# Kernel tuning notes

Measured on AMD Instinct MI355X. Metric: run time of the kernel, lower is better.

## Reference

```python
import jax, jax.numpy as jnp
import numpy as np

B, C, T = 256, 22, 1000          # batch, EEG channels, samples
NB, M, E, K = 6, 8, 6, 3         # nbands, m, num_experts, top_k
KERNELS = (3, 5, 7)
FS = 250
POOL = FS // 2                   # 125
NUM_CLASSES = 9
EPS = 1e-5
NUM_TAPS = 21


def _firwin_bp(numtaps, f1, f2, fs):
    """scipy.signal.firwin(numtaps,[f1,f2],pass_zero=False,fs=fs) with Hamming window."""
    nyq = fs / 2.0
    lo, hi = f1 / nyq, f2 / nyq
    m = np.arange(numtaps) - (numtaps - 1) / 2.0
    h = hi * np.sinc(hi * m) - lo * np.sinc(lo * m)
    h = h * np.hamming(numtaps)
    h = h / np.sum(h * np.cos(np.pi * m * (lo + hi) / 2.0))  # unit gain at band center
    return h.astype(np.float32)


def setup_inputs() -> dict:
    key = jax.random.key(0)
    ks = jax.random.split(key, 10)
    fir = np.stack([_firwin_bp(NUM_TAPS, lo, lo + 4, FS) for lo in range(8, 32, 4)])  # (6,21)
    return {
        "x": jax.random.normal(ks[0], (B, C, T), jnp.float32),
        "fir_kernels": jnp.asarray(fir),
        "pconv_w3": jax.random.normal(ks[1], (NB, 1, 1, 3), jnp.float32) * 0.3,
        "pconv_w5": jax.random.normal(ks[2], (NB, 1, 1, 5), jnp.float32) * 0.3,
        "pconv_w7": jax.random.normal(ks[3], (NB, 1, 1, 7), jnp.float32) * 0.3,
        "bn1_g": jnp.ones((NB,), jnp.float32),
        "bn1_b": jnp.zeros((NB,), jnp.float32),
        "bn1_m": jnp.zeros((NB,), jnp.float32),
        "bn1_v": jnp.ones((NB,), jnp.float32),
        "sconv_w": jax.random.normal(ks[4], (NB, 1, C, 1), jnp.float32) * 0.2,
        "gate_w": jax.random.normal(ks[5], (M * NB, NB), jnp.float32) * 0.4,
        "gate_b": jnp.zeros((M * NB,), jnp.float32),
        "exp_w": jax.random.normal(ks[6], (E, M * NB, NB), jnp.float32) * 0.3,
        "exp_b": jnp.zeros((E, M * NB), jnp.float32),
        "ebn_g": jnp.ones((E, M * NB), jnp.float32),
        "ebn_b": jnp.zeros((E, M * NB), jnp.float32),
        "ebn_m": jnp.zeros((E, M * NB), jnp.float32),
        "ebn_v": jnp.ones((E, M * NB), jnp.float32),
        "fc_w": jax.random.normal(ks[7], (NUM_CLASSES, M * NB * (T // POOL)), jnp.float32) * 0.05,
        "fc_b": jnp.zeros((NUM_CLASSES,), jnp.float32),
    }


def _forward(x, fir_kernels, pconv_w3, pconv_w5, pconv_w7, bn1_g, bn1_b, bn1_m, bn1_v,
             sconv_w, gate_w, gate_b, exp_w, exp_b, ebn_g, ebn_b, ebn_m, ebn_v, fc_w, fc_b):
    Bsz = x.shape[0]
    pad = NUM_TAPS // 2
    # --- FIR filterbank: depthwise conv1d, channel-multiplier = NB bands ---
    rhs = jnp.broadcast_to(fir_kernels[None, :, None, :], (C, NB, 1, NUM_TAPS)).reshape(C * NB, 1, NUM_TAPS)
    xb = jax.lax.conv_general_dilated(x, rhs, (1,), [(pad, pad)],
                                      dimension_numbers=("NCH", "OIH", "NCH"), feature_group_count=C)
    xb = xb.reshape(Bsz, C, NB, T).transpose(0, 2, 1, 3)  # (B, NB, C, T)
    # --- parallel depthwise (1,k) convs, concat along time, avgpool(1, nk) ---
    outs = []
    for w in (pconv_w3, pconv_w5, pconv_w7):
        k = w.shape[-1]
        outs.append(jax.lax.conv_general_dilated(xb, w, (1, 1), [(0, 0), (k // 2, k // 2)],
                                                 dimension_numbers=("NCHW", "OIHW", "NCHW"),
                                                 feature_group_count=NB))
    h = jnp.concatenate(outs, axis=-1)                       # (B, NB, C, nk*T)
    nk = len(KERNELS)
    h = h.reshape(Bsz, NB, C, h.shape[-1] // nk, nk).mean(-1)  # (B, NB, C, T)
    # --- sconv: BN2d(eval) + ReLU + (dropout=identity in eval) + depthwise (C,1) conv ---
    scale1 = bn1_g / jnp.sqrt(bn1_v + EPS)
    h = (h - bn1_m[None, :, None, None]) * scale1[None, :, None, None] + bn1_b[None, :, None, None]
    h = jax.nn.relu(h)
    h = jax.lax.conv_general_dilated(h, sconv_w, (1, 1), [(0, 0), (0, 0)],
                                     dimension_numbers=("NCHW", "OIHW", "NCHW"), feature_group_count=NB)
    h = h[:, :, 0, :]                                        # squeeze -> (B, NB, T)
    # --- MoE: gate over M*NB logits, top-k mask (no grad), only first E cols mix experts ---
    gw = jax.nn.softmax(h.mean(-1) @ gate_w.T + gate_b, axis=-1)  # (B, M*NB)
    _, idx = jax.lax.top_k(gw, K)
    mask = jnp.zeros_like(gw).at[jnp.arange(Bsz)[:, None], idx].set(1.0)
    mask = jax.lax.stop_gradient(mask)
    gw = gw * mask
    gw = gw / gw.sum(-1, keepdims=True)
    # dense experts: 1x1 conv + avgpool(POOL) + BN1d(eval) + ReLU, vectorized over experts
    y = jnp.einsum("bct,eoc->beot", h, exp_w) + exp_b[None, :, :, None]   # (B, E, M*NB, T)
    y = y.reshape(Bsz, E, M * NB, T // POOL, POOL).mean(-1)               # (B, E, M*NB, T//POOL)
    escale = ebn_g / jnp.sqrt(ebn_v + EPS)
    y = (y - ebn_m[None, :, :, None]) * escale[None, :, :, None] + ebn_b[None, :, :, None]
    y = jax.nn.relu(y)
    out = jnp.einsum("be,beot->bot", gw[:, :E], y)                        # (B, M*NB, T//POOL)
    feats = out.reshape(Bsz, -1)                                          # (B, 384)
    logp = jax.nn.log_softmax(feats @ fc_w.T + fc_b, axis=1)              # (B, 9)
    return feats, logp


def reference(x, fir_kernels, pconv_w3, pconv_w5, pconv_w7, bn1_g, bn1_b, bn1_m, bn1_v,
              sconv_w, gate_w, gate_b, exp_w, exp_b, ebn_g, ebn_b, ebn_m, ebn_v, fc_w, fc_b):
    return _forward(x, fir_kernels, pconv_w3, pconv_w5, pconv_w7, bn1_g, bn1_b, bn1_m, bn1_v,
                    sconv_w, gate_w, gate_b, exp_w, exp_b, ebn_g, ebn_b, ebn_m, ebn_v, fc_w, fc_b)
```

## Files before the change

### kernel.cpp

```cpp
#include <hip/hip_runtime.h>
#include <math.h>

#define B_    256
#define C_    22
#define T_    1000
#define NB_   6
#define E_    6
#define MNB_  48
#define POOL_ 125
#define TP_   8
#define NC_   9
#define FEAT_ 384

#define PQ_   352
#define NTH   768
#define CH_   11

#define PASS(OFF, KK)                                                        \
    {                                                                        \
        float f[16];                                                         \
        const float4* pb = (const float4*)(base + (OFF));                    \
        *(float4*)&f[0]  = pb[0]; *(float4*)&f[4]  = pb[1];                  \
        *(float4*)&f[8]  = pb[2]; *(float4*)&f[12] = pb[3];                  \
        _Pragma("unroll")                                                    \
        for (int u = 0; u < 13; ++u) {                                       \
            const float cj = ck2[KK][u];                                     \
            s0 = fmaf(cj, f[u    ], s0);                                     \
            s1 = fmaf(cj, f[u + 1], s1);                                     \
            s2 = fmaf(cj, f[u + 2], s2);                                     \
            s3 = fmaf(cj, f[u + 3], s3);                                     \
        }                                                                    \
    }

#define RUN_NB(NBV, A0, A1, A2, A3)                                          \
    {                                                                        \
        const int nbL = (NBV);                                               \
        float ck2[3][13];                                                    \
        _Pragma("unroll")                                                    \
        for (int k = 0; k < 3; ++k)                                          \
            _Pragma("unroll")                                                \
            for (int u = 0; u < 13; ++u) ck2[k][u] = ckl2[rr][nbL][k][u];    \
        const float sc3 = sbn6[nbL][0], bi = sbn6[nbL][1];                   \
        _Pragma("unroll 1")                                                  \
        for (int c = 0; c < CH_; ++c) {                                      \
            const float* base = &pl[c][0][0];                                \
            float s0 = 0.f, s1 = 0.f, s2 = 0.f, s3 = 0.f;                    \
            PASS(off0, 0)                                                    \
            PASS(off1, 1)                                                    \
            PASS(off2, 2)                                                    \
            const float sw = sws6[nbL][h * CH_ + c];                         \
            A0 += fmaxf(fmaf(s0, sc3, bi), 0.f) * sw;                        \
            A1 += fmaxf(fmaf(s1, sc3, bi), 0.f) * sw;                        \
            A2 += fmaxf(fmaf(s2, sc3, bi), 0.f) * sw;                        \
            A3 += fmaxf(fmaf(s3, sc3, bi), 0.f) * sw;                        \
        }                                                                    \
    }

__global__ __launch_bounds__(NTH) void fb_fused(
    const float* __restrict__ x,
    const float* __restrict__ fir,
    const float* __restrict__ w3,
    const float* __restrict__ w5,
    const float* __restrict__ w7,
    const float* __restrict__ bn_g, const float* __restrict__ bn_b,
    const float* __restrict__ bn_m, const float* __restrict__ bn_v,
    const float* __restrict__ sconv_w,
    const float* __restrict__ gate_w, const float* __restrict__ gate_b,
    const float* __restrict__ exp_w,  const float* __restrict__ exp_b,
    const float* __restrict__ ebn_g,  const float* __restrict__ ebn_b,
    const float* __restrict__ ebn_m,  const float* __restrict__ ebn_v,
    const float* __restrict__ fc_w,   const float* __restrict__ fc_b,
    float* __restrict__ feats_out, float* __restrict__ logp_out)
{
    const int b   = blockIdx.x;
    const int tid = threadIdx.x;

    __shared__ __align__(16) float pl[CH_][3][PQ_];
    __shared__ float firs6[NB_][21];
    __shared__ float w3s6[NB_][3], w5s6[NB_][5], w7s6[NB_][7];
    __shared__ float sws6[NB_][C_];
    __shared__ float sbn6[NB_][2];
    __shared__ float ckl2[3][NB_][3][13];
    __shared__ float xbv[NB_][CH_][13];
    __shared__ float term[NB_][6][C_];
    __shared__ float corr[NB_][6];
    __shared__ float psum[MNB_];
    __shared__ float hpl[MNB_];
    __shared__ float gms[NB_];
    __shared__ float lg[MNB_];
    __shared__ float gsh[E_];
    __shared__ float fsh[FEAT_];
    __shared__ float fpart[NC_][8];
    __shared__ float lo[NC_];

    float (*hrow)[T_] = (float (*)[T_])pl;

    const float* xbase = x + (size_t)b * (C_ * T_);

    if (tid < 126)                      { int nb=tid/21; firs6[nb][tid%21] = fir[tid]; }
    else if (tid >= 128 && tid < 146)   { int k=tid-128; w3s6[k/3][k%3] = w3[k]; }
    else if (tid >= 160 && tid < 190)   { int k=tid-160; w5s6[k/5][k%5] = w5[k]; }
    else if (tid >= 192 && tid < 234)   { int k=tid-192; w7s6[k/7][k%7] = w7[k]; }
    else if (tid >= 256 && tid < 388)   { int k=tid-256; sws6[k/C_][k%C_] = sconv_w[k]; }
    else if (tid >= 400 && tid < 406) {
        const int nb = tid - 400;
        float sc = bn_g[nb] * rsqrtf(bn_v[nb] + 1e-5f);
        sbn6[nb][0] = sc * (1.f/3.f);
        sbn6[nb][1] = bn_b[nb] - bn_m[nb] * sc;
    }

    const bool act  = (tid < 750);
    const int  tile = act ? (tid % 250) : 0;
    const int  nbA  = act ? (tid / 250) : 0;
    const int  nbB  = nbA + 3;
    const int  rr   = (tile <= 82) ? 0 : (tile <= 166) ? 1 : 2;

    const int PLN[3][3]  = {{2,0,1},{1,2,0},{0,1,2}};
    const int AOFF[3][3] = {{0,4,4},{-332,-332,-332},{-664,-664,-664}};
    const int off0 = PLN[rr][0]*PQ_ + 4*tile + AOFF[rr][0];
    const int off1 = PLN[rr][1]*PQ_ + 4*tile + AOFF[rr][1];
    const int off2 = PLN[rr][2]*PQ_ + 4*tile + AOFF[rr][2];

    float aA0=0.f, aA1=0.f, aA2=0.f, aA3=0.f;
    float aB0=0.f, aB1=0.f, aB2=0.f, aB3=0.f;

    #pragma unroll 1
    for (int h = 0; h < 2; ++h) {
        #pragma unroll
        for (int k = 0; k < 4; ++k) {
            const int idx = tid + k * NTH;
            if (idx < CH_ * 264) {
                const int cl = idx / 264, r2 = idx % 264;
                const int p  = r2 / 88,  q0 = (r2 % 88) * 4;
                const float* xr = xbase + (h * CH_ + cl) * T_;
                float v[4];
                #pragma unroll
                for (int i = 0; i < 4; ++i) {
                    const int m  = 3 * (q0 + i) + p - 24;
                    const int mc = m < 0 ? 0 : (m > 999 ? 999 : m);
                    const float val = xr[mc];
                    v[i] = ((unsigned)m < 1000u) ? val : 0.f;
                }
                *(float4*)&pl[cl][p][q0] = make_float4(v[0], v[1], v[2], v[3]);
            }
        }
        __syncthreads();

        if (h == 0 && tid < 702) {
            const int rr2 = tid / 234, r234 = tid % 234;
            const int nb  = r234 / 39, r39 = r234 % 39;
            const int k   = r39 / 13,  u   = r39 % 13;
            const int IDX0[3][3] = {{3,0,0},{2,2,3},{1,1,1}};
            const int jj = k + 3*u - 3*IDX0[rr2][k];
            float s = 0.f;
            if (jj >= 0 && jj < 29) {
                const float* wk = (rr2 == 0) ? w3s6[nb] : (rr2 == 1 ? w5s6[nb] : w7s6[nb]);
                const int K = (rr2 == 0) ? 3 : (rr2 == 1 ? 5 : 7), pk = K >> 1;
                #pragma unroll
                for (int oi = 0; oi < 9; ++oi) {
                    const int o = oi - 3;
                    float we = 0.f;
                    for (int kk = 0; kk < 7; ++kk) {
                        if (kk < K) {
                            const int jx = o + pk - kk;
                            if (jx >= 0 && jx < 3) we += wk[kk];
                        }
                    }
                    const int i = jj - oi;
                    if (i >= 0 && i < 21) s = fmaf(we, firs6[nb][i], s);
                }
            }
            ckl2[rr2][nb][k][u] = s;
        }
        for (int idx = tid; idx < NB_ * CH_ * 13; idx += NTH) {
            const int nb = idx / (CH_ * 13), r143 = idx % (CH_ * 13);
            const int cl = r143 / 13, pos = r143 % 13;
            const int m  = (pos < 7) ? pos : (987 + pos);
            int mm = m + 14;
            int q  = mm / 3, p = mm - 3 * q;
            float s = 0.f;
            #pragma unroll
            for (int i = 0; i < 21; ++i) {
                s = fmaf(firs6[nb][i], pl[cl][p][q], s);
                ++p; if (p == 3) { p = 0; ++q; }
            }
            xbv[nb][cl][pos] = s;
        }
        __syncthreads();

        if (tid < NB_ * 6 * CH_) {
            const int nb  = tid / (6 * CH_), r66 = tid % (6 * CH_);
            const int tix = r66 / CH_, cl = r66 % CH_;
            const float* X  = xbv[nb][cl];
            const float* W3 = w3s6[nb];
            const float* W5 = w5s6[nb];
            const float* W7 = w7s6[nb];
            float s;
            switch (tix) {
            case 0:
                s = W3[1]*X[0]+W3[2]*X[1]
                  + W3[0]*X[0]+W3[1]*X[1]+W3[2]*X[2]
                  + W3[0]*X[1]+W3[1]*X[2]+W3[2]*X[3];
                break;
            case 1:
                s = W3[0]*X[8]+W3[1]*X[9]+W3[2]*X[10]
                  + W3[0]*X[9]+W3[1]*X[10]+W3[2]*X[11]
                  + W3[0]*X[10]+W3[1]*X[11]+W3[2]*X[12];
                break;
            case 2:
                s = W3[0]*X[11]+W3[1]*X[12]
                  + W5[2]*X[0]+W5[3]*X[1]+W5[4]*X[2]
                  + W5[1]*X[0]+W5[2]*X[1]+W5[3]*X[2]+W5[4]*X[3];
                break;
            case 3:
                s = W5[0]*X[9]+W5[1]*X[10]+W5[2]*X[11]+W5[3]*X[12]
                  + W5[0]*X[10]+W5[1]*X[11]+W5[2]*X[12]
                  + W7[3]*X[0]+W7[4]*X[1]+W7[5]*X[2]+W7[6]*X[3];
                break;
            case 4:
                s = W7[2]*X[0]+W7[3]*X[1]+W7[4]*X[2]+W7[5]*X[3]+W7[6]*X[4]
                  + W7[1]*X[0]+W7[2]*X[1]+W7[3]*X[2]+W7[4]*X[3]+W7[5]*X[4]+W7[6]*X[5]
                  + W7[0]*X[0]+W7[1]*X[1]+W7[2]*X[2]+W7[3]*X[3]+W7[4]*X[4]+W7[5]*X[5]+W7[6]*X[6];
                break;
            default:
                s = W7[0]*X[7]+W7[1]*X[8]+W7[2]*X[9]+W7[3]*X[10]+W7[4]*X[11]+W7[5]*X[12]
                  + W7[0]*X[8]+W7[1]*X[9]+W7[2]*X[10]+W7[3]*X[11]+W7[4]*X[12]
                  + W7[0]*X[9]+W7[1]*X[10]+W7[2]*X[11]+W7[3]*X[12];
                break;
            }
            const float v = fmaxf(fmaf(s, sbn6[nb][0], sbn6[nb][1]), 0.f);
            term[nb][tix][h * CH_ + cl] = v * sws6[nb][h * CH_ + cl];
        }

        if (act) {
            RUN_NB(nbA, aA0, aA1, aA2, aA3)
            RUN_NB(nbB, aB0, aB1, aB2, aB3)
        }
        __syncthreads();
    }

    if (act) {
        *(float4*)&hrow[nbA][4*tile] = make_float4(aA0, aA1, aA2, aA3);
        *(float4*)&hrow[nbB][4*tile] = make_float4(aB0, aB1, aB2, aB3);
    }
    if (tid >= 704 && tid < 740) {
        const int k = tid - 704;
        const int nb = k / 6, tix = k % 6;
        float s = 0.f;
        for (int c = 0; c < C_; ++c) s += term[nb][tix][c];
        corr[nb][tix] = s;
    }
    __syncthreads();
    if (tid < 36) {
        const int nb = tid / 6, tix = tid % 6;
        const int t = (tix == 0) ? 0 :
                      (tix <= 2) ? (331 + tix) :
                      (tix <= 4) ? (663 + tix) : 999;
        hrow[nb][t] = corr[nb][tix];
    }
    __syncthreads();

    if (tid < 384) {
        const int w = tid >> 3, jj = tid & 7;
        const int nb = w >> 3, p = w & 7;
        float s = 0.f;
        for (int k = jj; k < POOL_; k += 8) s += hrow[nb][p*POOL_ + k];
        s += __shfl_down(s, 4, 8);
        s += __shfl_down(s, 2, 8);
        s += __shfl_down(s, 1, 8);
        if (jj == 0) { psum[w] = s; hpl[w] = s * (1.f / POOL_); }
    }
    __syncthreads();
    if (tid < NB_) {
        float s = 0.f;
        for (int p = 0; p < TP_; ++p) s += psum[tid*TP_ + p];
        gms[tid] = s * (1.f / T_);
    }
    __syncthreads();

    if (tid < MNB_) {
        float s = gate_b[tid];
        for (int c = 0; c < NB_; ++c) s += gms[c] * gate_w[tid*NB_ + c];
        lg[tid] = s;
    }
    __syncthreads();
    if (tid == 0) {
        float mx = lg[0];
        for (int i = 1; i < MNB_; ++i) mx = fmaxf(mx, lg[i]);
        for (int i = 0; i < MNB_; ++i) lg[i] = expf(lg[i] - mx);
        int i1 = 0, i2 = -1, i3 = -1;
        float b1 = -1.f, b2 = -1.f, b3 = -1.f;
        for (int i = 0; i < MNB_; ++i) if (lg[i] > b1) { b1 = lg[i]; i1 = i; }
        for (int i = 0; i < MNB_; ++i) if (i != i1 && lg[i] > b2) { b2 = lg[i]; i2 = i; }
        for (int i = 0; i < MNB_; ++i) if (i != i1 && i != i2 && lg[i] > b3) { b3 = lg[i]; i3 = i; }
        const float s3 = lg[i1] + lg[i2] + lg[i3];
        for (int jj = 0; jj < E_; ++jj) gsh[jj] = 0.f;
        if (i1 < E_) gsh[i1] = lg[i1] / s3;
        if (i2 < E_) gsh[i2] = lg[i2] / s3;
        if (i3 < E_) gsh[i3] = lg[i3] / s3;
    }
    __syncthreads();

    if (tid < FEAT_) {
        const int o = tid >> 3, p = tid & 7;
        float outv = 0.f;
        #pragma unroll
        for (int e = 0; e < E_; ++e) {
            const int eo = e*MNB_ + o;
            float acc = exp_b[eo];
            #pragma unroll
            for (int c = 0; c < NB_; ++c)
                acc += hpl[c*TP_ + p] * exp_w[eo*NB_ + c];
            const float esc = ebn_g[eo] * rsqrtf(ebn_v[eo] + 1e-5f);
            float v = fmaf(acc - ebn_m[eo], esc, ebn_b[eo]);
            v = fmaxf(v, 0.f);
            outv += gsh[e] * v;
        }
        fsh[tid] = outv;
        feats_out[b*FEAT_ + tid] = outv;
    }
    __syncthreads();

    if (tid < NC_ * 8) {
        const int cls = tid >> 3, part = tid & 7;
        float s = 0.f;
        const float* wr = fc_w + cls*FEAT_ + part*48;
        const float* fr = fsh + part*48;
        for (int i = 0; i < 48; ++i) s = fmaf(fr[i], wr[i], s);
        fpart[cls][part] = s;
    }
    __syncthreads();
    if (tid < NC_) {
        float s = fc_b[tid];
        for (int p = 0; p < 8; ++p) s += fpart[tid][p];
        lo[tid] = s;
    }
    __syncthreads();
    if (tid == 0) {
        float mx = lo[0];
        for (int k = 1; k < NC_; ++k) mx = fmaxf(mx, lo[k]);
        float Z = 0.f;
        for (int k = 0; k < NC_; ++k) Z += expf(lo[k] - mx);
        const float lse = mx + logf(Z);
        for (int k = 0; k < NC_; ++k) logp_out[b*NC_ + k] = lo[k] - lse;
    }
}

extern "C" void kernel_launch(void* const* d_in, const int* in_sizes, int n_in,
                              void* d_out, int out_size, void* d_ws, size_t ws_size,
                              hipStream_t stream) {
    const float* x       = (const float*)d_in[0];
    const float* fir     = (const float*)d_in[1];
    const float* w3      = (const float*)d_in[2];
    const float* w5      = (const float*)d_in[3];
    const float* w7      = (const float*)d_in[4];
    const float* bn1_g   = (const float*)d_in[5];
    const float* bn1_b   = (const float*)d_in[6];
    const float* bn1_m   = (const float*)d_in[7];
    const float* bn1_v   = (const float*)d_in[8];
    const float* sconv_w = (const float*)d_in[9];
    const float* gate_w  = (const float*)d_in[10];
    const float* gate_b  = (const float*)d_in[11];
    const float* exp_w   = (const float*)d_in[12];
    const float* exp_b   = (const float*)d_in[13];
    const float* ebn_g   = (const float*)d_in[14];
    const float* ebn_b   = (const float*)d_in[15];
    const float* ebn_m   = (const float*)d_in[16];
    const float* ebn_v   = (const float*)d_in[17];
    const float* fc_w    = (const float*)d_in[18];
    const float* fc_b    = (const float*)d_in[19];

    float* out       = (float*)d_out;
    float* feats_out = out;
    float* logp_out  = out + B_ * FEAT_;

    fb_fused<<<B_, NTH, 0, stream>>>(x, fir, w3, w5, w7,
                                     bn1_g, bn1_b, bn1_m, bn1_v, sconv_w,
                                     gate_w, gate_b, exp_w, exp_b,
                                     ebn_g, ebn_b, ebn_m, ebn_v,
                                     fc_w, fc_b, feats_out, logp_out);
}
```

Measured before the change: 62.88 us.

## Trim zero-padded taps and make thread-to-tile mapping wavefront-uniform per region

Replaces the padded 3x13 per-plane coefficient layout with a compact 29-tap array and unrolls only the nonzero taps per plane (10/10/9 instead of 13/13/13), cutting the FMA count in the inner convolution loop. Thread mapping is changed so each group of 256 threads handles one region (rr), making the rr branch uniform across wavefronts and letting the compiler specialize the loads with constant offsets. This adds three code paths, which raises code size and possibly register use.

```diff
diff --git a/kernel.cpp b/kernel.cpp
--- a/kernel.cpp
+++ b/kernel.cpp
@@ -16,39 +16,49 @@
 #define NTH   768
 #define CH_   11
 
-#define PASS(OFF, KK)                                                        \
+#define LOADP(F, pp, Aoff)                                                   \
     {                                                                        \
-        float f[16];                                                         \
-        const float4* pb = (const float4*)(base + (OFF));                    \
-        *(float4*)&f[0]  = pb[0]; *(float4*)&f[4]  = pb[1];                  \
-        *(float4*)&f[8]  = pb[2]; *(float4*)&f[12] = pb[3];                  \
-        _Pragma("unroll")                                                    \
-        for (int u = 0; u < 13; ++u) {                                       \
-            const float cj = ck2[KK][u];                                     \
-            s0 = fmaf(cj, f[u    ], s0);                                     \
-            s1 = fmaf(cj, f[u + 1], s1);                                     \
-            s2 = fmaf(cj, f[u + 2], s2);                                     \
-            s3 = fmaf(cj, f[u + 3], s3);                                     \
-        }                                                                    \
+        const float4* pb = (const float4*)&bw[pp][4*tile + (Aoff)];          \
+        *(float4*)&F[0]  = pb[0]; *(float4*)&F[4]  = pb[1];                  \
+        *(float4*)&F[8]  = pb[2]; *(float4*)&F[12] = pb[3];                  \
+    }
+
+#define TAPS(F, idx0, j0, nj)                                                \
+    _Pragma("unroll")                                                        \
+    for (int a = 0; a < (nj); ++a) {                                         \
+        const float cj = ck[(j0) + 3*a];                                     \
+        s0 = fmaf(cj, F[(idx0) + a    ], s0);                                \
+        s1 = fmaf(cj, F[(idx0) + a + 1], s1);                                \
+        s2 = fmaf(cj, F[(idx0) + a + 2], s2);                                \
+        s3 = fmaf(cj, F[(idx0) + a + 3], s3);                                \
     }
 
 #define RUN_NB(NBV, A0, A1, A2, A3)                                          \
     {                                                                        \
-        const int nbL = (NBV);                                               \
-        float ck2[3][13];                                                    \
+        const int nbL_ = (NBV);                                              \
+        float ck[29];                                                        \
         _Pragma("unroll")                                                    \
-        for (int k = 0; k < 3; ++k)                                          \
-            _Pragma("unroll")                                                \
-            for (int u = 0; u < 13; ++u) ck2[k][u] = ckl2[rr][nbL][k][u];    \
-        const float sc3 = sbn6[nbL][0], bi = sbn6[nbL][1];                   \
+        for (int t2 = 0; t2 < 29; ++t2) ck[t2] = ckl[rr][nbL_][t2];          \
+        const float sc3 = sbn6[nbL_][0], bi = sbn6[nbL_][1];                 \
         _Pragma("unroll 1")                                                  \
         for (int c = 0; c < CH_; ++c) {                                      \
-            const float* base = &pl[c][0][0];                                \
+            const float (*bw)[PQ_] = pl[c];                                  \
+            float f0[16], f1[16], f2[16];                                    \
             float s0 = 0.f, s1 = 0.f, s2 = 0.f, s3 = 0.f;                    \
-            PASS(off0, 0)                                                    \
-            PASS(off1, 1)                                                    \
-            PASS(off2, 2)                                                    \
-            const float sw = sws6[nbL][h * CH_ + c];                         \
+            if (rr == 0) {                                                   \
+                LOADP(f0, 2, 0)    TAPS(f0, 3, 0, 10)                        \
+                LOADP(f1, 0, 4)    TAPS(f1, 0, 1, 10)                        \
+                LOADP(f2, 1, 4)    TAPS(f2, 0, 2, 9)                         \
+            } else if (rr == 1) {                                            \
+                LOADP(f0, 1, -332) TAPS(f0, 2, 0, 10)                        \
+                LOADP(f1, 2, -332) TAPS(f1, 2, 1, 10)                        \
+                LOADP(f2, 0, -332) TAPS(f2, 3, 2, 9)                         \
+            } else {                                                         \
+                LOADP(f0, 0, -664) TAPS(f0, 1, 0, 10)                        \
+                LOADP(f1, 1, -664) TAPS(f1, 1, 1, 10)                        \
+                LOADP(f2, 2, -664) TAPS(f2, 1, 2, 9)                         \
+            }                                                                \
+            const float sw = sws6[nbL_][h * CH_ + c];                        \
             A0 += fmaxf(fmaf(s0, sc3, bi), 0.f) * sw;                        \
             A1 += fmaxf(fmaf(s1, sc3, bi), 0.f) * sw;                        \
             A2 += fmaxf(fmaf(s2, sc3, bi), 0.f) * sw;                        \
@@ -80,7 +90,7 @@
     __shared__ float w3s6[NB_][3], w5s6[NB_][5], w7s6[NB_][7];
     __shared__ float sws6[NB_][C_];
     __shared__ float sbn6[NB_][2];
-    __shared__ float ckl2[3][NB_][3][13];
+    __shared__ float ckl[3][NB_][29];
     __shared__ float xbv[NB_][CH_][13];
     __shared__ float term[NB_][6][C_];
     __shared__ float corr[NB_][6];
@@ -109,17 +119,15 @@
         sbn6[nb][1] = bn_b[nb] - bn_m[nb] * sc;
     }
 
-    const bool act  = (tid < 750);
-    const int  tile = act ? (tid % 250) : 0;
-    const int  nbA  = act ? (tid / 250) : 0;
-    const int  nbB  = nbA + 3;
-    const int  rr   = (tile <= 82) ? 0 : (tile <= 166) ? 1 : 2;
-
-    const int PLN[3][3]  = {{2,0,1},{1,2,0},{0,1,2}};
-    const int AOFF[3][3] = {{0,4,4},{-332,-332,-332},{-664,-664,-664}};
-    const int off0 = PLN[rr][0]*PQ_ + 4*tile + AOFF[rr][0];
-    const int off1 = PLN[rr][1]*PQ_ + 4*tile + AOFF[rr][1];
-    const int off2 = PLN[rr][2]*PQ_ + 4*tile + AOFF[rr][2];
+    const int rr = tid >> 8;
+    const int j  = tid & 255;
+    int nbL = 0, tile = 0;
+    bool act = false;
+    if (rr == 0)      { act = (j < 249); nbL = j / 83; tile = j % 83; }
+    else if (rr == 1) { act = (j < 252); nbL = j / 84; tile = 83 + j % 84; }
+    else              { act = (j < 249); nbL = j / 83; tile = 167 + j % 83; }
+    const int nbA = nbL;
+    const int nbB = nbL + 3;
 
     float aA0=0.f, aA1=0.f, aA2=0.f, aA3=0.f;
     float aB0=0.f, aB1=0.f, aB2=0.f, aB3=0.f;
@@ -146,31 +154,26 @@
         }
         __syncthreads();
 
-        if (h == 0 && tid < 702) {
-            const int rr2 = tid / 234, r234 = tid % 234;
-            const int nb  = r234 / 39, r39 = r234 % 39;
-            const int k   = r39 / 13,  u   = r39 % 13;
-            const int IDX0[3][3] = {{3,0,0},{2,2,3},{1,1,1}};
-            const int jj = k + 3*u - 3*IDX0[rr2][k];
+        if (h == 0 && tid < 522) {
+            const int combo = tid / 29, jj = tid % 29;
+            const int rr2 = combo / 6, nb = combo % 6;
+            const float* wk = (rr2 == 0) ? w3s6[nb] : (rr2 == 1 ? w5s6[nb] : w7s6[nb]);
+            const int K = (rr2 == 0) ? 3 : (rr2 == 1 ? 5 : 7), pk = K >> 1;
             float s = 0.f;
-            if (jj >= 0 && jj < 29) {
-                const float* wk = (rr2 == 0) ? w3s6[nb] : (rr2 == 1 ? w5s6[nb] : w7s6[nb]);
-                const int K = (rr2 == 0) ? 3 : (rr2 == 1 ? 5 : 7), pk = K >> 1;
-                #pragma unroll
-                for (int oi = 0; oi < 9; ++oi) {
-                    const int o = oi - 3;
-                    float we = 0.f;
-                    for (int kk = 0; kk < 7; ++kk) {
-                        if (kk < K) {
-                            const int jx = o + pk - kk;
-                            if (jx >= 0 && jx < 3) we += wk[kk];
-                        }
+            #pragma unroll
+            for (int oi = 0; oi < 9; ++oi) {
+                const int o = oi - 3;
+                float we = 0.f;
+                for (int kk = 0; kk < 7; ++kk) {
+                    if (kk < K) {
+                        const int jx = o + pk - kk;
+                        if (jx >= 0 && jx < 3) we += wk[kk];
                     }
-                    const int i = jj - oi;
-                    if (i >= 0 && i < 21) s = fmaf(we, firs6[nb][i], s);
                 }
+                const int i = jj - oi;
+                if (i >= 0 && i < 21) s = fmaf(we, firs6[nb][i], s);
             }
-            ckl2[rr2][nb][k][u] = s;
+            ckl[rr2][nb][jj] = s;
         }
         for (int idx = tid; idx < NB_ * CH_ * 13; idx += NTH) {
             const int nb = idx / (CH_ * 13), r143 = idx % (CH_ * 13);
```

After: 115.3 us. 83.4% more time.
